# Performance work log

Measured on AMD Instinct MI355X. Metric: run time of the kernel, lower is better.

## Reference

```python
import jax, jax.numpy as jnp
import numpy as np

N_NODES = 100000
N_EDGES = 1600000
DIMS = [128, 128, 40]   # embedding_dim
SS_DIM = 64
DROP_P = 0.2


def setup_inputs() -> dict:
    key = jax.random.key(0)
    ks = jax.random.split(key, 8)
    x = jax.random.normal(ks[0], (N_NODES, DIMS[0]), dtype=jnp.float32)
    adj_row = jax.random.randint(ks[1], (N_EDGES,), 0, N_NODES)
    adj_col = jax.random.randint(ks[2], (N_EDGES,), 0, N_NODES)
    adj_val = jax.random.uniform(ks[3], (N_EDGES,), dtype=jnp.float32)
    # nn.Linear(in, out, bias=False): y = x @ W.T; store transposed as (in, out)
    def lin(k, fi, fo):
        b = 1.0 / np.sqrt(fi)
        return jax.random.uniform(k, (fi, fo), minval=-b, maxval=b, dtype=jnp.float32)
    W0 = lin(ks[4], DIMS[0], DIMS[1])
    W1 = lin(ks[5], DIMS[1], DIMS[2])
    Wss = lin(ks[6], DIMS[-2], SS_DIM)
    return {"x": x, "adj_row": adj_row, "adj_col": adj_col, "adj_val": adj_val,
            "W0": W0, "W1": W1, "Wss": Wss}


def reference(x, adj_row, adj_col, adj_val, W0, W1, Wss):
    N = x.shape[0]
    keep = 1.0 - DROP_P

    def spmm(h):  # sparse [N,N] @ dense [N,d] via gather + segment_sum
        return jax.ops.segment_sum(adj_val[:, None] * h[adj_col], adj_row,
                                   num_segments=N)

    # deterministic dropout masks (fixed key, training path val_test=False)
    k1, k2 = jax.random.split(jax.random.key(42))
    m1 = jax.random.bernoulli(k1, keep, (N, W0.shape[1]))
    m2 = jax.random.bernoulli(k2, keep, (N, W0.shape[1]))

    # main branch: ln=0 -> spmm, lin0, relu, dropout; ln=1 -> spmm, lin1
    h = jnp.where(m1, jax.nn.relu(spmm(x) @ W0) / keep, 0.0)
    h = spmm(h) @ W1

    # self-supervised branch: ln=0 -> spmm, lin0, relu, dropout; ln=1 -> spmm; classifier
    s = jnp.where(m2, jax.nn.relu(spmm(x) @ W0) / keep, 0.0)
    s = spmm(s) @ Wss
    return (h, s)
```

## Files before the change

kernel.cpp:

```cpp
#include <hip/hip_runtime.h>
#include <stdint.h>


#define NN 100000
#define NE 1600000
#define D 128
#define NW 400000
#define ZCP 128
#define DO1 40
#define DO2 64
#define OUT_S_OFF 4000000
#define KEEP_THR 6710886u
#define NB 49
#define CAP 36000
#define BINB 196
#define CONVB 12500
#define MASKB 3125
#define SPMMB 12500

typedef unsigned int uint;
typedef __attribute__((ext_vector_type(4))) float f32x4;
typedef __attribute__((ext_vector_type(8))) short short8;
union U4S8 { uint4 u; short8 s; };

__device__ __forceinline__ float bflo(uint p) { return __uint_as_float(p << 16); }
__device__ __forceinline__ float bfhi(uint p) { return __uint_as_float(p & 0xffff0000u); }
__device__ __forceinline__ uint f2bf(float f) {
  uint u = __float_as_uint(f);
  return (u + 0x7fffu + ((u >> 16) & 1u)) >> 16;
}
__device__ __forceinline__ uint pack2(float lo, float hi) {
  return f2bf(lo) | (f2bf(hi) << 16);
}

__device__ __forceinline__ void tf2x32(uint k0, uint k1, uint x0, uint x1,
                                       uint& o0, uint& o1) {
  uint ks2 = k0 ^ k1 ^ 0x1BD11BDAu;
  x0 += k0; x1 += k1;
#define TFR(r) { x0 += x1; x1 = (x1 << (r)) | (x1 >> (32 - (r))); x1 ^= x0; }
  TFR(13) TFR(15) TFR(26) TFR(6)
  x0 += k1;  x1 += ks2 + 1u;
  TFR(17) TFR(29) TFR(16) TFR(24)
  x0 += ks2; x1 += k0 + 2u;
  TFR(13) TFR(15) TFR(26) TFR(6)
  x0 += k0;  x1 += k1 + 3u;
  TFR(17) TFR(29) TFR(16) TFR(24)
  x0 += k1;  x1 += ks2 + 4u;
  TFR(13) TFR(15) TFR(26) TFR(6)
  x0 += ks2; x1 += k0 + 5u;
#undef TFR
  o0 = x0; o1 = x1;
}

__global__ void bin_conv_prep_kernel(const int* __restrict__ row, const int* __restrict__ col,
                                     const float* __restrict__ val, int* __restrict__ cursor,
                                     uint2* __restrict__ buck,
                                     const float* __restrict__ x, uint* __restrict__ xb,
                                     const float* __restrict__ W0, const float* __restrict__ W1,
                                     const float* __restrict__ Wss,
                                     ushort* __restrict__ w0t, ushort* __restrict__ wcatT) {
  int bid = blockIdx.x, tid = threadIdx.x;
  if (bid < BINB) {
    __shared__ int h[NB];
    __shared__ int base[NB];
    if (tid < NB) h[tid] = 0;
    __syncthreads();
    int e0 = bid * 8192;
#pragma unroll 4
    for (int j = 0; j < 32; ++j) {
      int e = e0 + j * 256 + tid;
      if (e < NE) atomicAdd(&h[row[e] >> 11], 1);
    }
    __syncthreads();
    if (tid < NB) {
      int c = h[tid];
      base[tid] = c ? (tid * CAP + atomicAdd(&cursor[tid], c)) : 0;
      h[tid] = 0;
    }
    __syncthreads();
#pragma unroll 4
    for (int j = 0; j < 32; ++j) {
      int e = e0 + j * 256 + tid;
      if (e < NE) {
        int r = row[e];
        int b = r >> 11;
        int k = atomicAdd(&h[b], 1);
        int idx = base[b] + k;
        int lim = (b + 1) * CAP;
        if (idx >= lim) idx = lim - 1;
        buck[idx] = make_uint2(((uint)(r & 2047) << 17) | (uint)col[e],
                               __float_as_uint(val[e]));
      }
    }
  } else if (bid < BINB + CONVB) {
    int i = (bid - BINB) * 256 + tid;
    float4 v = ((const float4*)x)[i];
    ((uint2*)xb)[i] = make_uint2(pack2(v.x, v.y), pack2(v.z, v.w));
  } else {
    int idx = (bid - BINB - CONVB) * 256 + tid;
    if (idx < 16384) {
      int c = idx >> 7, k = idx & 127;
      w0t[idx] = (ushort)f2bf(W0[k * D + c]);
    } else {
      int j = idx - 16384;
      int c = j >> 7, k = j & 127;
      float v = (c < 40) ? W1[k * DO1 + c] : ((c < 48) ? 0.f : Wss[k * DO2 + (c - 48)]);
      wcatT[j] = (ushort)f2bf(v);
    }
  }
}

__global__ __launch_bounds__(1024) void csr_kernel(
    const uint2* __restrict__ buck, const int* __restrict__ cursor,
    int* __restrict__ ptr, uint2* __restrict__ cv) {
  __shared__ int cnt[2048];
  __shared__ int sc[2048];
  __shared__ int cb[NB];
  int b = blockIdx.x, tid = threadIdx.x;
  if (tid < NB) cb[tid] = min(cursor[tid], CAP);
  int i0 = tid, i1 = tid + 1024;
  cnt[i0] = 0; cnt[i1] = 0;
  __syncthreads();
  int gbase = 0;
  for (int i = 0; i < b; ++i) gbase += cb[i];
  int n = cb[b];
  int src = b * CAP;
  for (int i = tid; i < n; i += 1024) atomicAdd(&cnt[buck[src + i].x >> 17], 1);
  __syncthreads();
  sc[i0] = cnt[i0]; sc[i1] = cnt[i1];
  __syncthreads();
  for (int off = 1; off < 2048; off <<= 1) {
    int v0 = (i0 >= off) ? sc[i0 - off] : 0;
    int v1 = (i1 >= off) ? sc[i1 - off] : 0;
    __syncthreads();
    sc[i0] += v0; sc[i1] += v1;
    __syncthreads();
  }
  int r0 = b * 2048;
  int s0 = sc[i0] - cnt[i0], s1 = sc[i1] - cnt[i1];
  if (r0 + i0 < NN) ptr[r0 + i0] = gbase + s0;
  if (r0 + i1 < NN) ptr[r0 + i1] = gbase + s1;
  if (b == 0 && tid == 0) ptr[NN] = NE;
  cnt[i0] = s0; cnt[i1] = s1;
  __syncthreads();
  for (int i = tid; i < n; i += 1024) {
    uint2 e = buck[src + i];
    int rl = e.x >> 17;
    int k = atomicAdd(&cnt[rl], 1);
    cv[gbase + k] = make_uint2(e.x & 0x1FFFFu, e.y);
  }
}

__global__ void spmm_mask_kernel(const int* __restrict__ ptr, const uint2* __restrict__ cv,
                                 const uint2* __restrict__ xb, uint2* __restrict__ t,
                                 uint* __restrict__ m1, uint* __restrict__ m2) {
  int bid = blockIdx.x, tid = threadIdx.x;
  int q = bid / 5, rsel = bid % 5;
  if (rsel == 4) {
    int tt = q * 256 + tid;
    uint a0, a1, b0, b1;
    tf2x32(0u, 42u, 0u, 0u, a0, a1);
    tf2x32(0u, 42u, 0u, 1u, b0, b1);
    bool second = (tt >= NW);
    uint w  = second ? (uint)(tt - NW) : (uint)tt;
    uint k0 = second ? b0 : a0;
    uint k1 = second ? b1 : a1;
    uint base = w * 32u;
    uint word = 0u;
    for (int i = 0; i < 32; ++i) {
      uint o0, o1;
      tf2x32(k0, k1, 0u, base + (uint)i, o0, o1);
      word |= (uint)(((o0 ^ o1) >> 9) <= KEEP_THR) << i;
    }
    (second ? m2 : m1)[w] = word;
    return;
  }
  int sb = 4 * q + rsel;
  int r = sb * 8 + (tid >> 5);
  int k = tid & 31;
  int s = ptr[r], e = ptr[r + 1];
  float a0 = 0.f, a1 = 0.f, a2 = 0.f, a3 = 0.f;
  int i = s;
  for (; i + 8 <= e; i += 8) {
    uint2 ee[8], pp[8];
#pragma unroll
    for (int j = 0; j < 8; ++j) ee[j] = cv[i + j];
#pragma unroll
    for (int j = 0; j < 8; ++j) pp[j] = xb[ee[j].x * 32 + k];
#pragma unroll
    for (int j = 0; j < 8; ++j) {
      float v = __uint_as_float(ee[j].y);
      a0 += v * bflo(pp[j].x); a1 += v * bfhi(pp[j].x);
      a2 += v * bflo(pp[j].y); a3 += v * bfhi(pp[j].y);
    }
  }
  if (i + 4 <= e) {
    uint2 ee[4], pp[4];
#pragma unroll
    for (int j = 0; j < 4; ++j) ee[j] = cv[i + j];
#pragma unroll
    for (int j = 0; j < 4; ++j) pp[j] = xb[ee[j].x * 32 + k];
#pragma unroll
    for (int j = 0; j < 4; ++j) {
      float v = __uint_as_float(ee[j].y);
      a0 += v * bflo(pp[j].x); a1 += v * bfhi(pp[j].x);
      a2 += v * bflo(pp[j].y); a3 += v * bfhi(pp[j].y);
    }
    i += 4;
  }
  for (; i < e; ++i) {
    uint2 ev = cv[i];
    float v = __uint_as_float(ev.y);
    uint2 p = xb[ev.x * 32 + k];
    a0 += v * bflo(p.x); a1 += v * bfhi(p.x);
    a2 += v * bflo(p.y); a3 += v * bfhi(p.y);
  }
  t[r * 32 + k] = make_uint2(pack2(a0, a1), pack2(a2, a3));
}

#define SWZ(row, byte) ((row) * 256 + ((byte) ^ ((((row) >> 1) & 7) << 4)))
__global__ __launch_bounds__(512, 4) void pass_a_kernel(
    const uint* __restrict__ tb, const ushort* __restrict__ w0t,
    const ushort* __restrict__ wcatT,
    const uint* __restrict__ m1, const uint* __restrict__ m2,
    ushort* __restrict__ zz) {
  __shared__ __align__(16) char ldsb[69632];
  uint* mlds = (uint*)(ldsb + 65536);

  int t = threadIdx.x;
  int r0 = blockIdx.x * 128;
  int wid = t >> 6, l = t & 63, lc = l & 15, lk = l >> 4;

#pragma unroll
  for (int i = 0; i < 4; ++i) {
    int lin = i * 512 + t;
    int row = lin >> 4, seg = lin & 15;
    int gr = r0 + row;
    uint4 v = make_uint4(0, 0, 0, 0);
    if (gr < NN) v = ((const uint4*)(tb + (size_t)gr * 64))[seg];
    *(uint4*)&ldsb[SWZ(row, seg * 16)] = v;
    uint4 w = ((const uint4*)w0t)[lin];
    *(uint4*)&ldsb[32768 + SWZ(row, seg * 16)] = w;
  }
#pragma unroll
  for (int i = 0; i < 2; ++i) {
    int idx = t;
    int row = idx >> 2, word = idx & 3;
    int gr = r0 + row;
    uint v = 0;
    if (gr < NN) v = (i == 0 ? m1 : m2)[gr * 4 + word];
    mlds[i * 512 + idx] = v;
  }
  __syncthreads();

  short8 af[4];
#pragma unroll
  for (int s = 0; s < 4; ++s) {
    U4S8 tmp; tmp.u = *(uint4*)&ldsb[SWZ(16 * wid + lc, 64 * s + 16 * lk)];
    af[s] = tmp.s;
  }
  f32x4 acc[8];
#pragma unroll
  for (int n = 0; n < 8; ++n) acc[n] = (f32x4)(0.f);
#pragma unroll
  for (int n = 0; n < 8; ++n) {
#pragma unroll
    for (int s = 0; s < 4; ++s) {
      U4S8 tmp; tmp.u = *(uint4*)&ldsb[32768 + SWZ(16 * n + lc, 64 * s + 16 * lk)];
      acc[n] = __builtin_amdgcn_mfma_f32_16x16x32_bf16(af[s], tmp.s, acc[n], 0, 0, 0);
    }
  }
  __syncthreads();

#pragma unroll
  for (int reg = 0; reg < 4; ++reg) {
    int row = 16 * wid + 4 * lk + reg;
    uint4 w1q = *(uint4*)&mlds[row * 4];
    uint4 w2q = *(uint4*)&mlds[512 + row * 4];
    uint w1a[4] = {w1q.x, w1q.y, w1q.z, w1q.w};
    uint w2a[4] = {w2q.x, w2q.y, w2q.z, w2q.w};
#pragma unroll
    for (int n = 0; n < 8; ++n) {
      float v = fmaxf(acc[n][reg], 0.f) * 1.25f;
      ushort ub = (ushort)f2bf(v);
      int bit = (n & 1) * 16 + lc;
      ushort u1 = ((w1a[n >> 1] >> bit) & 1u) ? ub : (ushort)0;
      ushort u2 = ((w2a[n >> 1] >> bit) & 1u) ? ub : (ushort)0;
      int ad = SWZ(row, 32 * n + 2 * lc);
      *(ushort*)&ldsb[ad] = u1;
      *(ushort*)&ldsb[32768 + ad] = u2;
    }
  }
  __syncthreads();

  f32x4 acc2[7];
#pragma unroll
  for (int n = 0; n < 7; ++n) acc2[n] = (f32x4)(0.f);
#pragma unroll
  for (int n2 = 0; n2 < 7; ++n2) {
    int ubase = (n2 < 3) ? 0 : 32768;
#pragma unroll
    for (int s = 0; s < 4; ++s) {
      U4S8 a2; a2.u = ((const uint4*)wcatT)[(16 * n2 + lc) * 16 + 4 * s + lk];
      U4S8 b2; b2.u = *(uint4*)&ldsb[ubase + SWZ(16 * wid + lc, 64 * s + 16 * lk)];
      acc2[n2] = __builtin_amdgcn_mfma_f32_16x16x32_bf16(a2.s, b2.s, acc2[n2], 0, 0, 0);
    }
  }

  int r = r0 + 16 * wid + lc;
  if (r < NN) {
#pragma unroll
    for (int n2 = 0; n2 < 7; ++n2) {
      if (n2 == 2 && lk >= 2) continue;
      int cb = 16 * n2 + 4 * lk;
      if (n2 >= 3) cb -= 8;
      uint2 v = make_uint2(pack2(acc2[n2][0], acc2[n2][1]),
                           pack2(acc2[n2][2], acc2[n2][3]));
      *(uint2*)(zz + (size_t)r * ZCP + cb) = v;
    }
  }
}

__global__ void gather_out_kernel(const int* __restrict__ ptr, const uint2* __restrict__ cv,
                                  const uint2* __restrict__ zp, float* __restrict__ out) {
  int r = blockIdx.x * 8 + (threadIdx.x >> 5);
  int k = threadIdx.x & 31;
  if (k >= 26) return;
  int s = ptr[r], e = ptr[r + 1];
  float a0 = 0.f, a1 = 0.f, a2 = 0.f, a3 = 0.f;
  int i = s;
  for (; i + 8 <= e; i += 8) {
    uint2 ee[8], pp[8];
#pragma unroll
    for (int j = 0; j < 8; ++j) ee[j] = cv[i + j];
#pragma unroll
    for (int j = 0; j < 8; ++j) pp[j] = zp[ee[j].x * 32 + k];
#pragma unroll
    for (int j = 0; j < 8; ++j) {
      float v = __uint_as_float(ee[j].y);
      a0 += v * bflo(pp[j].x); a1 += v * bfhi(pp[j].x);
      a2 += v * bflo(pp[j].y); a3 += v * bfhi(pp[j].y);
    }
  }
  if (i + 4 <= e) {
    uint2 ee[4], pp[4];
#pragma unroll
    for (int j = 0; j < 4; ++j) ee[j] = cv[i + j];
#pragma unroll
    for (int j = 0; j < 4; ++j) pp[j] = zp[ee[j].x * 32 + k];
#pragma unroll
    for (int j = 0; j < 4; ++j) {
      float v = __uint_as_float(ee[j].y);
      a0 += v * bflo(pp[j].x); a1 += v * bfhi(pp[j].x);
      a2 += v * bflo(pp[j].y); a3 += v * bfhi(pp[j].y);
    }
    i += 4;
  }
  for (; i < e; ++i) {
    uint2 ev = cv[i];
    float v = __uint_as_float(ev.y);
    uint2 p = zp[ev.x * 32 + k];
    a0 += v * bflo(p.x); a1 += v * bfhi(p.x);
    a2 += v * bflo(p.y); a3 += v * bfhi(p.y);
  }
  if (k < 10) {
    *(float4*)(out + (size_t)r * DO1 + 4 * k) = make_float4(a0, a1, a2, a3);
  } else {
    *(float4*)(out + OUT_S_OFF + (size_t)r * DO2 + 4 * (k - 10)) = make_float4(a0, a1, a2, a3);
  }
}

extern "C" void kernel_launch(void* const* d_in, const int* in_sizes, int n_in,
                              void* d_out, int out_size, void* d_ws, size_t ws_size,
                              hipStream_t stream) {
  const float* x       = (const float*)d_in[0];
  const int*   adj_row = (const int*)d_in[1];
  const int*   adj_col = (const int*)d_in[2];
  const float* adj_val = (const float*)d_in[3];
  const float* W0      = (const float*)d_in[4];
  const float* W1      = (const float*)d_in[5];
  const float* Wss     = (const float*)d_in[6];
  float* out = (float*)d_out;

  char* ws = (char*)d_ws;
  uint*   t_bf  = (uint*)(ws + 0);
  uint2*  buck  = (uint2*)(ws + 0);
  uint*   xb    = (uint*)(ws + 25600000);
  ushort* zz    = (ushort*)(ws + 25600000);
  uint*   m1    = (uint*)(ws + 51200000);
  uint*   m2    = (uint*)(ws + 52800000);
  int*    ptr   = (int*)(ws + 54400000);
  ushort* w0t   = (ushort*)(ws + 54800016);
  ushort* wcatT = (ushort*)(ws + 54832784);
  int*    curs  = (int*)(ws + 54861456);
  uint2*  cv    = (uint2*)(ws + 55600016);

  hipMemsetAsync(curs, 0, NB * sizeof(int), stream);
  bin_conv_prep_kernel<<<BINB + CONVB + 120, 256, 0, stream>>>(
      adj_row, adj_col, adj_val, curs, buck, x, xb, W0, W1, Wss, w0t, wcatT);
  csr_kernel<<<NB, 1024, 0, stream>>>(buck, curs, ptr, cv);
  spmm_mask_kernel<<<SPMMB + MASKB, 256, 0, stream>>>(ptr, cv, (const uint2*)xb,
                                                      (uint2*)t_bf, m1, m2);
  pass_a_kernel<<<782, 512, 0, stream>>>(t_bf, w0t, wcatT, m1, m2, zz);
  gather_out_kernel<<<12500, 256, 0, stream>>>(ptr, cv, (const uint2*)zz, out);
}
```

Before: 281.3 us.

## Move dropout mask generation into prep kernel and unroll gathers to 16

Dropout mask generation with Threefry moves out of the SpMM kernel and into the first prep kernel, where it is interleaved with the x-to-bf16 conversion blocks. The SpMM now runs as a plain per-row kernel without a mask branch. Both the SpMM gather loop and the output gather loop are unrolled to 16 edges per step, with the 8-edge step kept as a tail. The aim is to overlap mask work with memory-bound binning and conversion and to raise memory-level parallelism in the gathers, at the cost of higher register pressure and possibly lower occupancy.

```diff
diff --git a/kernel.cpp b/kernel.cpp
--- a/kernel.cpp
+++ b/kernel.cpp
@@ -16,7 +16,7 @@
 #define BINB 196
 #define CONVB 12500
 #define MASKB 3125
-#define SPMMB 12500
+#define WPREPB 120
 
 typedef unsigned int uint;
 typedef __attribute__((ext_vector_type(4))) float f32x4;
@@ -52,13 +52,15 @@
   o0 = x0; o1 = x1;
 }
 
-__global__ void bin_conv_prep_kernel(const int* __restrict__ row, const int* __restrict__ col,
-                                     const float* __restrict__ val, int* __restrict__ cursor,
-                                     uint2* __restrict__ buck,
-                                     const float* __restrict__ x, uint* __restrict__ xb,
-                                     const float* __restrict__ W0, const float* __restrict__ W1,
-                                     const float* __restrict__ Wss,
-                                     ushort* __restrict__ w0t, ushort* __restrict__ wcatT) {
+__global__ void bin_conv_mask_prep_kernel(
+    const int* __restrict__ row, const int* __restrict__ col,
+    const float* __restrict__ val, int* __restrict__ cursor,
+    uint2* __restrict__ buck,
+    const float* __restrict__ x, uint* __restrict__ xb,
+    uint* __restrict__ m1, uint* __restrict__ m2,
+    const float* __restrict__ W0, const float* __restrict__ W1,
+    const float* __restrict__ Wss,
+    ushort* __restrict__ w0t, ushort* __restrict__ wcatT) {
   int bid = blockIdx.x, tid = threadIdx.x;
   if (bid < BINB) {
     __shared__ int h[NB];
@@ -92,12 +94,33 @@
                                __float_as_uint(val[e]));
       }
     }
-  } else if (bid < BINB + CONVB) {
-    int i = (bid - BINB) * 256 + tid;
-    float4 v = ((const float4*)x)[i];
-    ((uint2*)xb)[i] = make_uint2(pack2(v.x, v.y), pack2(v.z, v.w));
+  } else if (bid < BINB + CONVB + MASKB) {
+    int u = bid - BINB;
+    int q = u / 5, rsel = u % 5;
+    if (rsel == 4) {
+      int tt = q * 256 + tid;
+      uint a0, a1, b0, b1;
+      tf2x32(0u, 42u, 0u, 0u, a0, a1);
+      tf2x32(0u, 42u, 0u, 1u, b0, b1);
+      bool second = (tt >= NW);
+      uint w  = second ? (uint)(tt - NW) : (uint)tt;
+      uint k0 = second ? b0 : a0;
+      uint k1 = second ? b1 : a1;
+      uint base = w * 32u;
+      uint word = 0u;
+      for (int i = 0; i < 32; ++i) {
+        uint o0, o1;
+        tf2x32(k0, k1, 0u, base + (uint)i, o0, o1);
+        word |= (uint)(((o0 ^ o1) >> 9) <= KEEP_THR) << i;
+      }
+      (second ? m2 : m1)[w] = word;
+    } else {
+      int i = (4 * q + rsel) * 256 + tid;
+      float4 v = ((const float4*)x)[i];
+      ((uint2*)xb)[i] = make_uint2(pack2(v.x, v.y), pack2(v.z, v.w));
+    }
   } else {
-    int idx = (bid - BINB - CONVB) * 256 + tid;
+    int idx = (bid - BINB - CONVB - MASKB) * 256 + tid;
     if (idx < 16384) {
       int c = idx >> 7, k = idx & 127;
       w0t[idx] = (ushort)f2bf(W0[k * D + c]);
@@ -151,37 +174,27 @@
   }
 }
 
-__global__ void spmm_mask_kernel(const int* __restrict__ ptr, const uint2* __restrict__ cv,
-                                 const uint2* __restrict__ xb, uint2* __restrict__ t,
-                                 uint* __restrict__ m1, uint* __restrict__ m2) {
-  int bid = blockIdx.x, tid = threadIdx.x;
-  int q = bid / 5, rsel = bid % 5;
-  if (rsel == 4) {
-    int tt = q * 256 + tid;
-    uint a0, a1, b0, b1;
-    tf2x32(0u, 42u, 0u, 0u, a0, a1);
-    tf2x32(0u, 42u, 0u, 1u, b0, b1);
-    bool second = (tt >= NW);
-    uint w  = second ? (uint)(tt - NW) : (uint)tt;
-    uint k0 = second ? b0 : a0;
-    uint k1 = second ? b1 : a1;
-    uint base = w * 32u;
-    uint word = 0u;
-    for (int i = 0; i < 32; ++i) {
-      uint o0, o1;
-      tf2x32(k0, k1, 0u, base + (uint)i, o0, o1);
-      word |= (uint)(((o0 ^ o1) >> 9) <= KEEP_THR) << i;
-    }
-    (second ? m2 : m1)[w] = word;
-    return;
-  }
-  int sb = 4 * q + rsel;
-  int r = sb * 8 + (tid >> 5);
-  int k = tid & 31;
+__global__ void spmm_x_kernel(const int* __restrict__ ptr, const uint2* __restrict__ cv,
+                              const uint2* __restrict__ xb, uint2* __restrict__ t) {
+  int r = blockIdx.x * 8 + (threadIdx.x >> 5);
+  int k = threadIdx.x & 31;
   int s = ptr[r], e = ptr[r + 1];
   float a0 = 0.f, a1 = 0.f, a2 = 0.f, a3 = 0.f;
   int i = s;
-  for (; i + 8 <= e; i += 8) {
+  for (; i + 16 <= e; i += 16) {
+    uint2 ee[16], pp[16];
+#pragma unroll
+    for (int j = 0; j < 16; ++j) ee[j] = cv[i + j];
+#pragma unroll
+    for (int j = 0; j < 16; ++j) pp[j] = xb[ee[j].x * 32 + k];
+#pragma unroll
+    for (int j = 0; j < 16; ++j) {
+      float v = __uint_as_float(ee[j].y);
+      a0 += v * bflo(pp[j].x); a1 += v * bfhi(pp[j].x);
+      a2 += v * bflo(pp[j].y); a3 += v * bfhi(pp[j].y);
+    }
+  }
+  if (i + 8 <= e) {
     uint2 ee[8], pp[8];
 #pragma unroll
     for (int j = 0; j < 8; ++j) ee[j] = cv[i + j];
@@ -193,6 +206,7 @@
       a0 += v * bflo(pp[j].x); a1 += v * bfhi(pp[j].x);
       a2 += v * bflo(pp[j].y); a3 += v * bfhi(pp[j].y);
     }
+    i += 8;
   }
   if (i + 4 <= e) {
     uint2 ee[4], pp[4];
@@ -329,7 +343,20 @@
   int s = ptr[r], e = ptr[r + 1];
   float a0 = 0.f, a1 = 0.f, a2 = 0.f, a3 = 0.f;
   int i = s;
-  for (; i + 8 <= e; i += 8) {
+  for (; i + 16 <= e; i += 16) {
+    uint2 ee[16], pp[16];
+#pragma unroll
+    for (int j = 0; j < 16; ++j) ee[j] = cv[i + j];
+#pragma unroll
+    for (int j = 0; j < 16; ++j) pp[j] = zp[ee[j].x * 32 + k];
+#pragma unroll
+    for (int j = 0; j < 16; ++j) {
+      float v = __uint_as_float(ee[j].y);
+      a0 += v * bflo(pp[j].x); a1 += v * bfhi(pp[j].x);
+      a2 += v * bflo(pp[j].y); a3 += v * bfhi(pp[j].y);
+    }
+  }
+  if (i + 8 <= e) {
     uint2 ee[8], pp[8];
 #pragma unroll
     for (int j = 0; j < 8; ++j) ee[j] = cv[i + j];
@@ -341,6 +368,7 @@
       a0 += v * bflo(pp[j].x); a1 += v * bfhi(pp[j].x);
       a2 += v * bflo(pp[j].y); a3 += v * bfhi(pp[j].y);
     }
+    i += 8;
   }
   if (i + 4 <= e) {
     uint2 ee[4], pp[4];
@@ -396,11 +424,10 @@
   uint2*  cv    = (uint2*)(ws + 55600016);
 
   hipMemsetAsync(curs, 0, NB * sizeof(int), stream);
-  bin_conv_prep_kernel<<<BINB + CONVB + 120, 256, 0, stream>>>(
-      adj_row, adj_col, adj_val, curs, buck, x, xb, W0, W1, Wss, w0t, wcatT);
+  bin_conv_mask_prep_kernel<<<BINB + CONVB + MASKB + WPREPB, 256, 0, stream>>>(
+      adj_row, adj_col, adj_val, curs, buck, x, xb, m1, m2, W0, W1, Wss, w0t, wcatT);
   csr_kernel<<<NB, 1024, 0, stream>>>(buck, curs, ptr, cv);
-  spmm_mask_kernel<<<SPMMB + MASKB, 256, 0, stream>>>(ptr, cv, (const uint2*)xb,
-                                                      (uint2*)t_bf, m1, m2);
+  spmm_x_kernel<<<12500, 256, 0, stream>>>(ptr, cv, (const uint2*)xb, (uint2*)t_bf);
   pass_a_kernel<<<782, 512, 0, stream>>>(t_bf, w0t, wcatT, m1, m2, zz);
   gather_out_kernel<<<12500, 256, 0, stream>>>(ptr, cv, (const uint2*)zz, out);
 }
```

Result: slower. 287.4 us (+2.2%).

## Split feature dims into column-slab layout for SpMM gathers and move mask generation

Applied to the files above, without the earlier changes.

Stores bf16 activations (x, intermediate t, and zz) in 8 feature slabs of 16 columns each, so each SpMM block handles one slab for 64 rows with 4 threads per row. Blocks are ordered so the 8 slabs of a row group are adjacent, which is meant to give each gathered slab better L2/cache locality (each slab is 3.2MB). Dropout mask generation moves from the SpMM kernel into the prep kernel, and pass_a and gather_out are reindexed for the new layout. The cost is that each row's edge list (ptr/cv) is re-read once per slab, and gather_out launches some blocks that do nothing.

```diff
diff --git a/kernel.cpp b/kernel.cpp
--- a/kernel.cpp
+++ b/kernel.cpp
@@ -6,7 +6,6 @@
 #define NE 1600000
 #define D 128
 #define NW 400000
-#define ZCP 128
 #define DO1 40
 #define DO2 64
 #define OUT_S_OFF 4000000
@@ -16,7 +15,8 @@
 #define BINB 196
 #define CONVB 12500
 #define MASKB 3125
-#define SPMMB 12500
+#define WPREPB 120
+#define NG 1563
 
 typedef unsigned int uint;
 typedef __attribute__((ext_vector_type(4))) float f32x4;
@@ -52,13 +52,15 @@
   o0 = x0; o1 = x1;
 }
 
-__global__ void bin_conv_prep_kernel(const int* __restrict__ row, const int* __restrict__ col,
-                                     const float* __restrict__ val, int* __restrict__ cursor,
-                                     uint2* __restrict__ buck,
-                                     const float* __restrict__ x, uint* __restrict__ xb,
-                                     const float* __restrict__ W0, const float* __restrict__ W1,
-                                     const float* __restrict__ Wss,
-                                     ushort* __restrict__ w0t, ushort* __restrict__ wcatT) {
+__global__ void bin_conv_mask_prep_kernel(
+    const int* __restrict__ row, const int* __restrict__ col,
+    const float* __restrict__ val, int* __restrict__ cursor,
+    uint2* __restrict__ buck,
+    const float* __restrict__ x, uint2* __restrict__ xbc,
+    uint* __restrict__ m1, uint* __restrict__ m2,
+    const float* __restrict__ W0, const float* __restrict__ W1,
+    const float* __restrict__ Wss,
+    ushort* __restrict__ w0t, ushort* __restrict__ wcatT) {
   int bid = blockIdx.x, tid = threadIdx.x;
   if (bid < BINB) {
     __shared__ int h[NB];
@@ -92,12 +94,36 @@
                                __float_as_uint(val[e]));
       }
     }
-  } else if (bid < BINB + CONVB) {
-    int i = (bid - BINB) * 256 + tid;
-    float4 v = ((const float4*)x)[i];
-    ((uint2*)xb)[i] = make_uint2(pack2(v.x, v.y), pack2(v.z, v.w));
+  } else if (bid < BINB + CONVB + MASKB) {
+    int u = bid - BINB;
+    int q = u / 5, rsel = u % 5;
+    if (rsel == 4) {
+      int tt = q * 256 + tid;
+      uint a0, a1, b0, b1;
+      tf2x32(0u, 42u, 0u, 0u, a0, a1);
+      tf2x32(0u, 42u, 0u, 1u, b0, b1);
+      bool second = (tt >= NW);
+      uint w  = second ? (uint)(tt - NW) : (uint)tt;
+      uint k0 = second ? b0 : a0;
+      uint k1 = second ? b1 : a1;
+      uint base = w * 32u;
+      uint word = 0u;
+      for (int i = 0; i < 32; ++i) {
+        uint o0, o1;
+        tf2x32(k0, k1, 0u, base + (uint)i, o0, o1);
+        word |= (uint)(((o0 ^ o1) >> 9) <= KEEP_THR) << i;
+      }
+      (second ? m2 : m1)[w] = word;
+    } else {
+      int i = (4 * q + rsel) * 256 + tid;
+      float4 v = ((const float4*)x)[i];
+      int rw = i >> 5, w = i & 31;
+      int f = w >> 2, w4 = w & 3;
+      xbc[(size_t)f * (NN * 4) + rw * 4 + w4] =
+          make_uint2(pack2(v.x, v.y), pack2(v.z, v.w));
+    }
   } else {
-    int idx = (bid - BINB - CONVB) * 256 + tid;
+    int idx = (bid - BINB - CONVB - MASKB) * 256 + tid;
     if (idx < 16384) {
       int c = idx >> 7, k = idx & 127;
       w0t[idx] = (ushort)f2bf(W0[k * D + c]);
@@ -151,71 +177,53 @@
   }
 }
 
-__global__ void spmm_mask_kernel(const int* __restrict__ ptr, const uint2* __restrict__ cv,
-                                 const uint2* __restrict__ xb, uint2* __restrict__ t,
-                                 uint* __restrict__ m1, uint* __restrict__ m2) {
-  int bid = blockIdx.x, tid = threadIdx.x;
-  int q = bid / 5, rsel = bid % 5;
-  if (rsel == 4) {
-    int tt = q * 256 + tid;
-    uint a0, a1, b0, b1;
-    tf2x32(0u, 42u, 0u, 0u, a0, a1);
-    tf2x32(0u, 42u, 0u, 1u, b0, b1);
-    bool second = (tt >= NW);
-    uint w  = second ? (uint)(tt - NW) : (uint)tt;
-    uint k0 = second ? b0 : a0;
-    uint k1 = second ? b1 : a1;
-    uint base = w * 32u;
-    uint word = 0u;
-    for (int i = 0; i < 32; ++i) {
-      uint o0, o1;
-      tf2x32(k0, k1, 0u, base + (uint)i, o0, o1);
-      word |= (uint)(((o0 ^ o1) >> 9) <= KEEP_THR) << i;
-    }
-    (second ? m2 : m1)[w] = word;
-    return;
-  }
-  int sb = 4 * q + rsel;
-  int r = sb * 8 + (tid >> 5);
-  int k = tid & 31;
+__global__ void spmm_x_kernel(const int* __restrict__ ptr, const uint2* __restrict__ cv,
+                              const uint2* __restrict__ xbc, uint2* __restrict__ tc) {
+  int bid = blockIdx.x;
+  int f = bid & 7, g = bid >> 3;
+  int tid = threadIdx.x;
+  int rl = tid >> 2, j = tid & 3;
+  int r = g * 64 + rl;
+  if (r >= NN) return;
+  const uint2* xf = xbc + (size_t)f * (NN * 4);
   int s = ptr[r], e = ptr[r + 1];
   float a0 = 0.f, a1 = 0.f, a2 = 0.f, a3 = 0.f;
   int i = s;
   for (; i + 8 <= e; i += 8) {
     uint2 ee[8], pp[8];
 #pragma unroll
-    for (int j = 0; j < 8; ++j) ee[j] = cv[i + j];
-#pragma unroll
-    for (int j = 0; j < 8; ++j) pp[j] = xb[ee[j].x * 32 + k];
-#pragma unroll
-    for (int j = 0; j < 8; ++j) {
-      float v = __uint_as_float(ee[j].y);
-      a0 += v * bflo(pp[j].x); a1 += v * bfhi(pp[j].x);
-      a2 += v * bflo(pp[j].y); a3 += v * bfhi(pp[j].y);
+    for (int q = 0; q < 8; ++q) ee[q] = cv[i + q];
+#pragma unroll
+    for (int q = 0; q < 8; ++q) pp[q] = xf[ee[q].x * 4 + j];
+#pragma unroll
+    for (int q = 0; q < 8; ++q) {
+      float v = __uint_as_float(ee[q].y);
+      a0 += v * bflo(pp[q].x); a1 += v * bfhi(pp[q].x);
+      a2 += v * bflo(pp[q].y); a3 += v * bfhi(pp[q].y);
     }
   }
   if (i + 4 <= e) {
     uint2 ee[4], pp[4];
 #pragma unroll
-    for (int j = 0; j < 4; ++j) ee[j] = cv[i + j];
-#pragma unroll
-    for (int j = 0; j < 4; ++j) pp[j] = xb[ee[j].x * 32 + k];
-#pragma unroll
-    for (int j = 0; j < 4; ++j) {
-      float v = __uint_as_float(ee[j].y);
-      a0 += v * bflo(pp[j].x); a1 += v * bfhi(pp[j].x);
-      a2 += v * bflo(pp[j].y); a3 += v * bfhi(pp[j].y);
+    for (int q = 0; q < 4; ++q) ee[q] = cv[i + q];
+#pragma unroll
+    for (int q = 0; q < 4; ++q) pp[q] = xf[ee[q].x * 4 + j];
+#pragma unroll
+    for (int q = 0; q < 4; ++q) {
+      float v = __uint_as_float(ee[q].y);
+      a0 += v * bflo(pp[q].x); a1 += v * bfhi(pp[q].x);
+      a2 += v * bflo(pp[q].y); a3 += v * bfhi(pp[q].y);
     }
     i += 4;
   }
   for (; i < e; ++i) {
     uint2 ev = cv[i];
     float v = __uint_as_float(ev.y);
-    uint2 p = xb[ev.x * 32 + k];
+    uint2 p = xf[ev.x * 4 + j];
     a0 += v * bflo(p.x); a1 += v * bfhi(p.x);
     a2 += v * bflo(p.y); a3 += v * bfhi(p.y);
   }
-  t[r * 32 + k] = make_uint2(pack2(a0, a1), pack2(a2, a3));
+  tc[(size_t)f * (NN * 4) + r * 4 + j] = make_uint2(pack2(a0, a1), pack2(a2, a3));
 }
 
 #define SWZ(row, byte) ((row) * 256 + ((byte) ^ ((((row) >> 1) & 7) << 4)))
@@ -234,13 +242,15 @@
 #pragma unroll
   for (int i = 0; i < 4; ++i) {
     int lin = i * 512 + t;
-    int row = lin >> 4, seg = lin & 15;
+    int f = lin >> 8, rh = lin & 255;
+    int row = rh >> 1, half = rh & 1;
     int gr = r0 + row;
     uint4 v = make_uint4(0, 0, 0, 0);
-    if (gr < NN) v = ((const uint4*)(tb + (size_t)gr * 64))[seg];
-    *(uint4*)&ldsb[SWZ(row, seg * 16)] = v;
+    if (gr < NN) v = ((const uint4*)tb)[(size_t)f * (NN * 2) + gr * 2 + half];
+    *(uint4*)&ldsb[SWZ(row, f * 32 + half * 16)] = v;
+    int row2 = lin >> 4, seg2 = lin & 15;
     uint4 w = ((const uint4*)w0t)[lin];
-    *(uint4*)&ldsb[32768 + SWZ(row, seg * 16)] = w;
+    *(uint4*)&ldsb[32768 + SWZ(row2, seg2 * 16)] = w;
   }
 #pragma unroll
   for (int i = 0; i < 2; ++i) {
@@ -314,59 +324,67 @@
       if (n2 == 2 && lk >= 2) continue;
       int cb = 16 * n2 + 4 * lk;
       if (n2 >= 3) cb -= 8;
+      int f = cb >> 4, woff = cb & 15;
       uint2 v = make_uint2(pack2(acc2[n2][0], acc2[n2][1]),
                            pack2(acc2[n2][2], acc2[n2][3]));
-      *(uint2*)(zz + (size_t)r * ZCP + cb) = v;
+      *(uint2*)(zz + (size_t)f * (NN * 16) + (size_t)r * 16 + woff) = v;
     }
   }
 }
 
 __global__ void gather_out_kernel(const int* __restrict__ ptr, const uint2* __restrict__ cv,
                                   const uint2* __restrict__ zp, float* __restrict__ out) {
-  int r = blockIdx.x * 8 + (threadIdx.x >> 5);
-  int k = threadIdx.x & 31;
-  if (k >= 26) return;
+  int bid = blockIdx.x;
+  int f = bid & 7, g = bid >> 3;
+  if (f == 7) return;
+  int tid = threadIdx.x;
+  int rl = tid >> 2, j = tid & 3;
+  int c = 16 * f + 4 * j;
+  if (c >= 104) return;
+  int r = g * 64 + rl;
+  if (r >= NN) return;
+  const uint2* zf = zp + (size_t)f * (NN * 4);
   int s = ptr[r], e = ptr[r + 1];
   float a0 = 0.f, a1 = 0.f, a2 = 0.f, a3 = 0.f;
   int i = s;
   for (; i + 8 <= e; i += 8) {
     uint2 ee[8], pp[8];
 #pragma unroll
-    for (int j = 0; j < 8; ++j) ee[j] = cv[i + j];
-#pragma unroll
-    for (int j = 0; j < 8; ++j) pp[j] = zp[ee[j].x * 32 + k];
-#pragma unroll
-    for (int j = 0; j < 8; ++j) {
-      float v = __uint_as_float(ee[j].y);
-      a0 += v * bflo(pp[j].x); a1 += v * bfhi(pp[j].x);
-      a2 += v * bflo(pp[j].y); a3 += v * bfhi(pp[j].y);
+    for (int q = 0; q < 8; ++q) ee[q] = cv[i + q];
+#pragma unroll
+    for (int q = 0; q < 8; ++q) pp[q] = zf[ee[q].x * 4 + j];
+#pragma unroll
+    for (int q = 0; q < 8; ++q) {
+      float v = __uint_as_float(ee[q].y);
+      a0 += v * bflo(pp[q].x); a1 += v * bfhi(pp[q].x);
+      a2 += v * bflo(pp[q].y); a3 += v * bfhi(pp[q].y);
     }
   }
   if (i + 4 <= e) {
     uint2 ee[4], pp[4];
 #pragma unroll
-    for (int j = 0; j < 4; ++j) ee[j] = cv[i + j];
-#pragma unroll
-    for (int j = 0; j < 4; ++j) pp[j] = zp[ee[j].x * 32 + k];
-#pragma unroll
-    for (int j = 0; j < 4; ++j) {
-      float v = __uint_as_float(ee[j].y);
-      a0 += v * bflo(pp[j].x); a1 += v * bfhi(pp[j].x);
-      a2 += v * bflo(pp[j].y); a3 += v * bfhi(pp[j].y);
+    for (int q = 0; q < 4; ++q) ee[q] = cv[i + q];
+#pragma unroll
+    for (int q = 0; q < 4; ++q) pp[q] = zf[ee[q].x * 4 + j];
+#pragma unroll
+    for (int q = 0; q < 4; ++q) {
+      float v = __uint_as_float(ee[q].y);
+      a0 += v * bflo(pp[q].x); a1 += v * bfhi(pp[q].x);
+      a2 += v * bflo(pp[q].y); a3 += v * bfhi(pp[q].y);
     }
     i += 4;
   }
   for (; i < e; ++i) {
     uint2 ev = cv[i];
     float v = __uint_as_float(ev.y);
-    uint2 p = zp[ev.x * 32 + k];
+    uint2 p = zf[ev.x * 4 + j];
     a0 += v * bflo(p.x); a1 += v * bfhi(p.x);
     a2 += v * bflo(p.y); a3 += v * bfhi(p.y);
   }
-  if (k < 10) {
-    *(float4*)(out + (size_t)r * DO1 + 4 * k) = make_float4(a0, a1, a2, a3);
+  if (c < DO1) {
+    *(float4*)(out + (size_t)r * DO1 + c) = make_float4(a0, a1, a2, a3);
   } else {
-    *(float4*)(out + OUT_S_OFF + (size_t)r * DO2 + 4 * (k - 10)) = make_float4(a0, a1, a2, a3);
+    *(float4*)(out + OUT_S_OFF + (size_t)r * DO2 + (c - DO1)) = make_float4(a0, a1, a2, a3);
   }
 }
 
@@ -385,7 +403,7 @@
   char* ws = (char*)d_ws;
   uint*   t_bf  = (uint*)(ws + 0);
   uint2*  buck  = (uint2*)(ws + 0);
-  uint*   xb    = (uint*)(ws + 25600000);
+  uint2*  xbc   = (uint2*)(ws + 25600000);
   ushort* zz    = (ushort*)(ws + 25600000);
   uint*   m1    = (uint*)(ws + 51200000);
   uint*   m2    = (uint*)(ws + 52800000);
@@ -396,11 +414,10 @@
   uint2*  cv    = (uint2*)(ws + 55600016);
 
   hipMemsetAsync(curs, 0, NB * sizeof(int), stream);
-  bin_conv_prep_kernel<<<BINB + CONVB + 120, 256, 0, stream>>>(
-      adj_row, adj_col, adj_val, curs, buck, x, xb, W0, W1, Wss, w0t, wcatT);
+  bin_conv_mask_prep_kernel<<<BINB + CONVB + MASKB + WPREPB, 256, 0, stream>>>(
+      adj_row, adj_col, adj_val, curs, buck, x, xbc, m1, m2, W0, W1, Wss, w0t, wcatT);
   csr_kernel<<<NB, 1024, 0, stream>>>(buck, curs, ptr, cv);
-  spmm_mask_kernel<<<SPMMB + MASKB, 256, 0, stream>>>(ptr, cv, (const uint2*)xb,
-                                                      (uint2*)t_bf, m1, m2);
+  spmm_x_kernel<<<8 * NG, 256, 0, stream>>>(ptr, cv, xbc, (uint2*)t_bf);
   pass_a_kernel<<<782, 512, 0, stream>>>(t_bf, w0t, wcatT, m1, m2, zz);
-  gather_out_kernel<<<12500, 256, 0, stream>>>(ptr, cv, (const uint2*)zz, out);
-}
+  gather_out_kernel<<<8 * NG, 256, 0, stream>>>(ptr, cv, (const uint2*)zz, out);
+}
```

New measurement: 353.1 us. 25.5% more time.
